# Kernel optimization log

Hardware: AMD Instinct MI355X
Metric: run time of the kernel (lower is better)

Reference implementation:

```python
import jax, jax.numpy as jnp
import numpy as np


def setup_inputs() -> dict:
    key = jax.random.key(0)
    ks = jax.random.split(key, 16)
    B, P, ENC = 128, 196, 2048          # batch, num pixels (14x14), encoder feature size
    E = D = A = 512                      # embed, decoder(hidden), attention sizes
    V, L = 10000, 52                     # vocab, max caption length
    s = 0.02
    rn = lambda k, shp: jax.random.normal(k, shp, jnp.float32) * s
    return {
        "features": jax.random.normal(ks[0], (B, P, ENC), jnp.float32),
        "captions": jax.random.randint(ks[1], (B, L), 0, V),
        "caption_lengths": jax.random.randint(ks[2], (B, 1), 2, L + 1),
        "emb": jax.random.uniform(ks[3], (V, E), jnp.float32, -0.1, 0.1),
        "W_enc_att": rn(ks[4], (ENC, A)), "b_enc_att": jnp.zeros((A,), jnp.float32),
        "W_dec_att": rn(ks[5], (D, A)),   "b_dec_att": jnp.zeros((A,), jnp.float32),
        "w_full": rn(ks[6], (A,)),        "b_full": jnp.zeros((), jnp.float32),
        "W_h0": rn(ks[7], (ENC, D)),      "b_h0": jnp.zeros((D,), jnp.float32),
        "W_c0": rn(ks[8], (ENC, D)),      "b_c0": jnp.zeros((D,), jnp.float32),
        "W_beta": rn(ks[9], (D, ENC)),    "b_beta": jnp.zeros((ENC,), jnp.float32),
        "W_ih": rn(ks[10], (E + ENC, 4 * D)), "b_ih": jnp.zeros((4 * D,), jnp.float32),
        "W_hh": rn(ks[11], (D, 4 * D)),       "b_hh": jnp.zeros((4 * D,), jnp.float32),
        "W_fc": jax.random.uniform(ks[12], (D, V), jnp.float32, -0.1, 0.1),
        "b_fc": jnp.zeros((V,), jnp.float32),
    }


def reference(features, captions, caption_lengths, emb,
              W_enc_att, b_enc_att, W_dec_att, b_dec_att, w_full, b_full,
              W_h0, b_h0, W_c0, b_c0, W_beta, b_beta,
              W_ih, b_ih, W_hh, b_hh, W_fc, b_fc):
    lens = caption_lengths[:, 0]
    order = jnp.argsort(-lens)                       # sort descending by length (stable)
    features = features[order]
    captions = captions[order]
    decode_lengths = lens[order] - 1                 # [B]
    T = captions.shape[1] - 1                        # static max decode length

    emb_seq = emb[captions[:, :T]]                   # [B,T,E]
    eo = features.mean(axis=1)                       # [B,ENC]
    h = eo @ W_h0 + b_h0                             # [B,D]
    c = eo @ W_c0 + b_c0
    enc_proj = features @ W_enc_att + b_enc_att      # [B,P,A] (precomputed, h-independent)

    def step(carry, xs):
        h, c = carry
        t, e_t = xs                                  # e_t: [B,E]
        mask = (decode_lengths > t)[:, None].astype(h.dtype)  # rows still decoding
        dec_proj = h @ W_dec_att + b_dec_att         # [B,A]
        scores = jax.nn.relu(enc_proj + dec_proj[:, None, :]) @ w_full + b_full  # [B,P]
        alpha = jax.nn.softmax(scores, axis=-1)      # [B,P]
        attw = jnp.einsum('bp,bpe->be', alpha, features)       # attention-weighted enc
        gate = jax.nn.sigmoid(h @ W_beta + b_beta)   # [B,ENC]
        x = jnp.concatenate([e_t, gate * attw], axis=1)        # [B,E+ENC]
        gates = x @ W_ih + b_ih + h @ W_hh + b_hh    # [B,4D], torch LSTMCell order i,f,g,o
        i, f, g, o = jnp.split(gates, 4, axis=1)
        c_new = jax.nn.sigmoid(f) * c + jax.nn.sigmoid(i) * jnp.tanh(g)
        h_new = jax.nn.sigmoid(o) * jnp.tanh(c_new)
        preds = h_new @ W_fc + b_fc                  # dropout is identity in eval
        h = mask * h_new + (1.0 - mask) * h          # freeze finished rows
        c = mask * c_new + (1.0 - mask) * c
        return (h, c), (preds * mask, alpha * mask)

    (_, _), (preds, alphas) = jax.lax.scan(
        step, (h, c), (jnp.arange(T), jnp.swapaxes(emb_seq, 0, 1)))
    predictions = jnp.swapaxes(preds, 0, 1)          # [B,T,V]
    alphas = jnp.swapaxes(alphas, 0, 1)              # [B,T,P]
    return predictions, captions, decode_lengths, alphas
```

## Files before the change

kernel.cpp:

```cpp
#include <hip/hip_runtime.h>
#include <math.h>

#define NB 128
#define NP 196
#define NENC 2048
#define NE 512
#define ND 512
#define NA 512
#define NV 10000
#define NVPAD 10112
#define NL 52
#define NT 51
#define KXH2 2560

typedef unsigned short u16;
typedef __attribute__((ext_vector_type(8))) short bf16x8;
typedef __attribute__((ext_vector_type(8))) unsigned short u16x8;
typedef __attribute__((ext_vector_type(4))) float f32x4;

#define MFMA16 __builtin_amdgcn_mfma_f32_16x16x32_bf16

__device__ __forceinline__ float sigmoidf_(float v) { return 1.0f / (1.0f + __expf(-v)); }
__device__ __forceinline__ float b2f(u16 u) { return __uint_as_float(((unsigned int)u) << 16); }
__device__ __forceinline__ u16 f2b(float f) {
  unsigned int u = __float_as_uint(f);
  unsigned int r = (u + 0x7FFFu + ((u >> 16) & 1u)) >> 16;
  return (u16)r;
}

__global__ void kSort(const int* __restrict__ cap_len, const int* __restrict__ captions,
                      int* __restrict__ order, int* __restrict__ nact,
                      float* __restrict__ out_cap, float* __restrict__ out_dlen) {
  __shared__ int lens[NB];
  __shared__ int s_dl[NB];
  int tid = threadIdx.x;
  lens[tid] = cap_len[tid];
  __syncthreads();
  int li = lens[tid];
  int r = 0;
  for (int j = 0; j < NB; ++j) {
    int lj = lens[j];
    if (lj > li || (lj == li && j < tid)) r++;
  }
  order[r] = tid;
  s_dl[r] = li - 1;
  out_dlen[r] = (float)(li - 1);
  for (int l = 0; l < NL; ++l)
    out_cap[(size_t)r * NL + l] = (float)captions[(size_t)tid * NL + l];
  __syncthreads();
  if (tid < NT) {
    int cnt = 0;
    for (int j = 0; j < NB; ++j) cnt += (s_dl[j] > tid) ? 1 : 0;
    nact[tid] = cnt;
  }
}

__global__ void kAlphaZero(const int* __restrict__ nact, float* __restrict__ out_alph) {
  int t = blockIdx.x;
  int n0 = nact[t];
  int cnt = (NB - n0) * NP;
  for (int i = threadIdx.x; i < cnt; i += 256) {
    int b = n0 + i / NP;
    int p = i - (i / NP) * NP;
    out_alph[((size_t)b * NT + t) * NP + p] = 0.0f;
  }
}

__global__ void kFeats(const float* __restrict__ features, const int* __restrict__ order,
                       u16* __restrict__ featsb) {
  int p = blockIdx.x, b = blockIdx.y, tid = threadIdx.x;
  const float* src = features + ((size_t)order[b] * NP + p) * NENC + tid * 8;
  u16* dst = featsb + ((size_t)b * NP + p) * NENC + tid * 8;
  float4 v0 = *(const float4*)src;
  float4 v1 = *(const float4*)(src + 4);
  u16x8 o;
  o[0] = f2b(v0.x); o[1] = f2b(v0.y); o[2] = f2b(v0.z); o[3] = f2b(v0.w);
  o[4] = f2b(v1.x); o[5] = f2b(v1.y); o[6] = f2b(v1.z); o[7] = f2b(v1.w);
  *(u16x8*)dst = o;
}

__device__ __forceinline__ float tfetch(int mode, int k, int n,
                                        const float* __restrict__ A,
                                        const float* __restrict__ B) {
  switch (mode) {
    case 0: return A[(size_t)k * NA + n];
    case 1: return (n < NA) ? A[(size_t)k * NA + n] : B[(size_t)k * NENC + (n - NA)];
    case 2: return A[(size_t)k * (4 * ND) + (n & 3) * ND + (n >> 2)];
    case 3: {
      int col = (n & 3) * ND + (n >> 2);
      return (k < NENC) ? A[(size_t)(NE + k) * (4 * ND) + col]
                        : B[(size_t)(k - NENC) * (4 * ND) + col];
    }
    case 4: return (n < NV) ? A[(size_t)k * NV + n] : 0.0f;
    default: return (n < NA) ? A[(size_t)k * ND + n] : B[(size_t)k * ND + (n - NA)];
  }
}

__global__ __launch_bounds__(256) void kTrans(const float* __restrict__ A,
                                              const float* __restrict__ B,
                                              u16* __restrict__ dst,
                                              int K, int N, int mode) {
  __shared__ u16 T[32][136];
  int n0 = blockIdx.x * 32, k0 = blockIdx.y * 128;
  int tid = threadIdx.x;
  int c = tid & 31, kr = tid >> 5;
#pragma unroll
  for (int pass = 0; pass < 16; ++pass) {
    int kl = pass * 8 + kr;
    T[c][kl] = f2b(tfetch(mode, k0 + kl, n0 + c, A, B));
  }
  __syncthreads();
  int row = tid >> 3, seg = tid & 7;
  u16x8 v0, v1;
#pragma unroll
  for (int j = 0; j < 8; ++j) { v0[j] = T[row][seg * 16 + j]; v1[j] = T[row][seg * 16 + 8 + j]; }
  *(u16x8*)&dst[(size_t)(n0 + row) * K + k0 + seg * 16] = v0;
  *(u16x8*)&dst[(size_t)(n0 + row) * K + k0 + seg * 16 + 8] = v1;
}

__global__ void kEmbA(const float* __restrict__ emb, const int* __restrict__ captions,
                      const int* __restrict__ order, u16* __restrict__ embA) {
  int t = blockIdx.x, b = blockIdx.y;
  int tok = captions[(size_t)order[b] * NL + t];
  int i = threadIdx.x * 2;
  float2 v = *(const float2*)(emb + (size_t)tok * NE + i);
  unsigned int w0 = (unsigned int)f2b(v.x) | ((unsigned int)f2b(v.y) << 16);
  *(unsigned int*)(embA + ((size_t)t * NB + b) * NE + i) = w0;
}

__global__ __launch_bounds__(256) void kEmbGemm(const u16* __restrict__ A,
                                                const u16* __restrict__ BT,
                                                u16* __restrict__ D) {
  int w = threadIdx.x >> 6, lane = threadIdx.x & 63;
  int lr = lane & 15, lg = lane >> 4;
  int mb = blockIdx.y * 128 + w * 32;
  int nb = blockIdx.x * 64;
  f32x4 acc[2][4] = {};
  const u16* a0 = A + (size_t)(mb + lr) * NE + lg * 8;
  const u16* a1 = a0 + 16 * NE;
  const u16* b0 = BT + (size_t)(nb + lr) * NE + lg * 8;
  for (int k0 = 0; k0 < NE; k0 += 32) {
    bf16x8 af0 = *(const bf16x8*)(a0 + k0);
    bf16x8 af1 = *(const bf16x8*)(a1 + k0);
#pragma unroll
    for (int nt = 0; nt < 4; ++nt) {
      bf16x8 bf = *(const bf16x8*)(b0 + (size_t)nt * 16 * NE + k0);
      acc[0][nt] = MFMA16(af0, bf, acc[0][nt], 0, 0, 0);
      acc[1][nt] = MFMA16(af1, bf, acc[1][nt], 0, 0, 0);
    }
  }
#pragma unroll
  for (int mt = 0; mt < 2; ++mt)
#pragma unroll
    for (int nt = 0; nt < 4; ++nt)
#pragma unroll
      for (int j = 0; j < 4; ++j) {
        int row = mb + mt * 16 + lg * 4 + j;
        int col = nb + nt * 16 + lr;
        D[(size_t)row * NENC + col] = f2b(acc[mt][nt][j]);
      }
}

__global__ void kEo(const u16* __restrict__ featsb, u16* __restrict__ eob) {
  int e = blockIdx.x * 256 + threadIdx.x;
  int b = blockIdx.y;
  const u16* f = featsb + (size_t)b * NP * NENC + e;
  float s = 0.0f;
  for (int p = 0; p < NP; ++p) s += b2f(f[(size_t)p * NENC]);
  eob[(size_t)b * NENC + e] = f2b(s * (1.0f / NP));
}

__global__ __launch_bounds__(64) void kHC0(const u16* __restrict__ eob,
                                           const u16* __restrict__ BT,
                                           const float* __restrict__ b_h0,
                                           const float* __restrict__ b_c0,
                                           u16* __restrict__ hb, u16* __restrict__ xh0,
                                           float* __restrict__ c) {
  int lane = threadIdx.x;
  int lr = lane & 15, lg = lane >> 4;
  int mb = blockIdx.y * 32, nb = blockIdx.x * 32;
  f32x4 acc[2][2] = {};
  const u16* a0 = eob + (size_t)(mb + lr) * NENC + lg * 8;
  const u16* a1 = a0 + 16 * NENC;
  const u16* b0 = BT + (size_t)(nb + lr) * NENC + lg * 8;
  const u16* b1 = b0 + 16 * NENC;
#pragma unroll 4
  for (int k0 = 0; k0 < NENC; k0 += 32) {
    bf16x8 af0 = *(const bf16x8*)(a0 + k0);
    bf16x8 af1 = *(const bf16x8*)(a1 + k0);
    bf16x8 bv0 = *(const bf16x8*)(b0 + k0);
    bf16x8 bv1 = *(const bf16x8*)(b1 + k0);
    acc[0][0] = MFMA16(af0, bv0, acc[0][0], 0, 0, 0);
    acc[1][0] = MFMA16(af1, bv0, acc[1][0], 0, 0, 0);
    acc[0][1] = MFMA16(af0, bv1, acc[0][1], 0, 0, 0);
    acc[1][1] = MFMA16(af1, bv1, acc[1][1], 0, 0, 0);
  }
#pragma unroll
  for (int mt = 0; mt < 2; ++mt)
#pragma unroll
    for (int nt = 0; nt < 2; ++nt)
#pragma unroll
      for (int j = 0; j < 4; ++j) {
        int row = mb + mt * 16 + lg * 4 + j;
        int n = nb + nt * 16 + lr;
        if (n < NA) {
          u16 hv = f2b(acc[mt][nt][j] + b_h0[n]);
          hb[(size_t)row * ND + n] = hv;
          xh0[(size_t)row * KXH2 + NENC + n] = hv;
        } else {
          c[(size_t)row * ND + (n - NA)] = acc[mt][nt][j] + b_c0[n - NA];
        }
      }
}

__global__ __launch_bounds__(256) void kEncProj(const u16* __restrict__ A,
                                                const u16* __restrict__ BT,
                                                const float* __restrict__ bias,
                                                u16* __restrict__ D) {
  __shared__ u16 As[2][128][72];
  int bid = blockIdx.x;
  int mt = bid >> 2, ntile = bid & 3;
  int mb = mt * 128, nb = ntile * 128;
  int tid = threadIdx.x;
  int w = tid >> 6, lane = tid & 63;
  int lr = lane & 15, lg = lane >> 4;

  int arow[4], akp[4];
  const u16* aptr[4];
#pragma unroll
  for (int i = 0; i < 4; ++i) {
    int idx = i * 256 + tid;
    arow[i] = idx >> 3;
    akp[i] = idx & 7;
    aptr[i] = A + (size_t)(mb + arow[i]) * NENC + akp[i] * 8;
  }
  u16x8 s0 = *(const u16x8*)(aptr[0]);
  u16x8 s1 = *(const u16x8*)(aptr[1]);
  u16x8 s2 = *(const u16x8*)(aptr[2]);
  u16x8 s3 = *(const u16x8*)(aptr[3]);
  *(u16x8*)&As[0][arow[0]][akp[0] * 8] = s0;
  *(u16x8*)&As[0][arow[1]][akp[1] * 8] = s1;
  *(u16x8*)&As[0][arow[2]][akp[2] * 8] = s2;
  *(u16x8*)&As[0][arow[3]][akp[3] * 8] = s3;

  f32x4 acc[2][8] = {};
  const u16* bbase = BT + (size_t)(nb + lr) * NENC + lg * 8;
  int cur = 0;
  int r0 = w * 32 + lr;

  for (int k0 = 0; k0 < NENC; k0 += 64) {
    __syncthreads();
    bool more = (k0 + 64 < NENC);
    if (more) {
      s0 = *(const u16x8*)(aptr[0] + k0 + 64);
      s1 = *(const u16x8*)(aptr[1] + k0 + 64);
      s2 = *(const u16x8*)(aptr[2] + k0 + 64);
      s3 = *(const u16x8*)(aptr[3] + k0 + 64);
    }
#pragma unroll
    for (int kh = 0; kh < 2; ++kh) {
      bf16x8 af0 = *(const bf16x8*)&As[cur][r0][kh * 32 + lg * 8];
      bf16x8 af1 = *(const bf16x8*)&As[cur][r0 + 16][kh * 32 + lg * 8];
#pragma unroll
      for (int nt = 0; nt < 8; ++nt) {
        bf16x8 bf = *(const bf16x8*)(bbase + (size_t)nt * 16 * NENC + k0 + kh * 32);
        acc[0][nt] = MFMA16(af0, bf, acc[0][nt], 0, 0, 0);
        acc[1][nt] = MFMA16(af1, bf, acc[1][nt], 0, 0, 0);
      }
    }
    if (more) {
      *(u16x8*)&As[cur ^ 1][arow[0]][akp[0] * 8] = s0;
      *(u16x8*)&As[cur ^ 1][arow[1]][akp[1] * 8] = s1;
      *(u16x8*)&As[cur ^ 1][arow[2]][akp[2] * 8] = s2;
      *(u16x8*)&As[cur ^ 1][arow[3]][akp[3] * 8] = s3;
    }
    cur ^= 1;
  }
  __syncthreads();
  u16* eps = (u16*)As;
#pragma unroll
  for (int m2 = 0; m2 < 2; ++m2)
#pragma unroll
    for (int nt = 0; nt < 8; ++nt)
#pragma unroll
      for (int j = 0; j < 4; ++j) {
        int rloc = w * 32 + m2 * 16 + lg * 4 + j;
        int col = nt * 16 + lr;
        eps[rloc * 136 + col] = f2b(acc[m2][nt][j] + bias[nb + col]);
      }
  __syncthreads();
#pragma unroll
  for (int i = 0; i < 8; ++i) {
    int idx = i * 256 + tid;
    int row = idx >> 4, seg = idx & 15;
    *(u16x8*)&D[(size_t)(mb + row) * NA + nb + seg * 8] = *(u16x8*)&eps[row * 136 + seg * 8];
  }
}

__global__ __launch_bounds__(64) void kDecGate(const u16* __restrict__ hb,
                                               const u16* __restrict__ BT,
                                               const float* __restrict__ b_dec,
                                               const float* __restrict__ b_beta,
                                               const int* __restrict__ nact, int t,
                                               float* __restrict__ dec_proj,
                                               float* __restrict__ gate_raw) {
  int nact_t = nact[t];
  int mb = blockIdx.y * 32;
  if (mb >= nact_t) return;
  int lane = threadIdx.x;
  int lr = lane & 15, lg = lane >> 4;
  int nb = blockIdx.x * 32;
  f32x4 acc[2][2] = {};
  const u16* a0 = hb + (size_t)(mb + lr) * ND + lg * 8;
  const u16* a1 = a0 + 16 * ND;
  const u16* b0 = BT + (size_t)(nb + lr) * ND + lg * 8;
  const u16* b1 = b0 + 16 * ND;
#pragma unroll 4
  for (int k0 = 0; k0 < ND; k0 += 32) {
    bf16x8 af0 = *(const bf16x8*)(a0 + k0);
    bf16x8 af1 = *(const bf16x8*)(a1 + k0);
    bf16x8 bv0 = *(const bf16x8*)(b0 + k0);
    bf16x8 bv1 = *(const bf16x8*)(b1 + k0);
    acc[0][0] = MFMA16(af0, bv0, acc[0][0], 0, 0, 0);
    acc[1][0] = MFMA16(af1, bv0, acc[1][0], 0, 0, 0);
    acc[0][1] = MFMA16(af0, bv1, acc[0][1], 0, 0, 0);
    acc[1][1] = MFMA16(af1, bv1, acc[1][1], 0, 0, 0);
  }
#pragma unroll
  for (int mt = 0; mt < 2; ++mt)
#pragma unroll
    for (int nt = 0; nt < 2; ++nt)
#pragma unroll
      for (int j = 0; j < 4; ++j) {
        int row = mb + mt * 16 + lg * 4 + j;
        int n = nb + nt * 16 + lr;
        if (n < NA)
          dec_proj[(size_t)row * NA + n] = acc[mt][nt][j] + b_dec[n];
        else
          gate_raw[(size_t)row * NENC + (n - NA)] = acc[mt][nt][j] + b_beta[n - NA];
      }
}

__global__ __launch_bounds__(256) void kSAX(const u16* __restrict__ featsb,
                                            const u16* __restrict__ encb,
                                            const float* __restrict__ dec_proj,
                                            const float* __restrict__ gate_raw,
                                            const float* __restrict__ w_full,
                                            const float* __restrict__ b_full,
                                            const int* __restrict__ nact, int t,
                                            u16* __restrict__ xh_w,
                                            float* __restrict__ out_alph) {
  int b = blockIdx.x, r = blockIdx.y, tid = threadIdx.x;
  if (b >= nact[t]) return;
  __shared__ float s_dp[NA], s_wf[NA], s_al[NP + 12], red[16];
  for (int i = tid; i < NA; i += 256) { s_dp[i] = dec_proj[(size_t)b * NA + i]; s_wf[i] = w_full[i]; }
  __syncthreads();
  int wave = tid >> 6, lane = tid & 63;
  float bf_ = b_full[0];
  for (int p = wave; p < NP; p += 4) {
    const u16* ep = encb + ((size_t)b * NP + p) * NA + lane * 8;
    u16x8 v = *(const u16x8*)ep;
    float acc = 0.0f;
#pragma unroll
    for (int j = 0; j < 8; ++j) {
      int a = lane * 8 + j;
      float vv = b2f(v[j]) + s_dp[a];
      acc += fmaxf(vv, 0.0f) * s_wf[a];
    }
#pragma unroll
    for (int off = 32; off; off >>= 1) acc += __shfl_down(acc, off);
    if (lane == 0) s_al[p] = acc + bf_;
  }
  __syncthreads();
  float mx = -3.4e38f;
  for (int p = tid; p < NP; p += 256) mx = fmaxf(mx, s_al[p]);
#pragma unroll
  for (int off = 32; off; off >>= 1) mx = fmaxf(mx, __shfl_down(mx, off));
  if (lane == 0) red[wave] = mx;
  __syncthreads();
  if (tid == 0) red[0] = fmaxf(fmaxf(red[0], red[1]), fmaxf(red[2], red[3]));
  __syncthreads();
  float m2v = red[0];
  float sm = 0.0f;
  for (int p = tid; p < NP; p += 256) { float e = __expf(s_al[p] - m2v); s_al[p] = e; sm += e; }
#pragma unroll
  for (int off = 32; off; off >>= 1) sm += __shfl_down(sm, off);
  if (lane == 0) red[8 + wave] = sm;
  __syncthreads();
  if (tid == 0) red[8] = 1.0f / (red[8] + red[9] + red[10] + red[11]);
  __syncthreads();
  float inv = red[8];
  for (int p = tid; p < NP; p += 256) {
    float al = s_al[p] * inv;
    s_al[p] = al;
    if (r == 0) out_alph[((size_t)b * NT + t) * NP + p] = al;
  }
  __syncthreads();
  int e0 = r * 512 + tid * 2;
  float ac0 = 0.0f, ac1 = 0.0f;
  const u16* fb = featsb + (size_t)b * NP * NENC + e0;
#pragma unroll 4
  for (int p = 0; p < NP; ++p) {
    unsigned int v = *(const unsigned int*)(fb + (size_t)p * NENC);
    float al = s_al[p];
    ac0 += al * __uint_as_float(v << 16);
    ac1 += al * __uint_as_float(v & 0xffff0000u);
  }
  float g0 = sigmoidf_(gate_raw[(size_t)b * NENC + e0]);
  float g1 = sigmoidf_(gate_raw[(size_t)b * NENC + e0 + 1]);
  unsigned int wo = (unsigned int)f2b(ac0 * g0) | ((unsigned int)f2b(ac1 * g1) << 16);
  *(unsigned int*)(xh_w + (size_t)b * KXH2 + e0) = wo;
}

__global__ __launch_bounds__(1024) void kGatesLstm(const u16* __restrict__ xh_r,
                                                   const u16* __restrict__ WifgoT2,
                                                   const u16* __restrict__ embAll,
                                                   const float* __restrict__ b_ih,
                                                   const float* __restrict__ b_hh,
                                                   const int* __restrict__ nact, int t,
                                                   float* __restrict__ cst,
                                                   u16* __restrict__ hb,
                                                   u16* __restrict__ hnewAll_t,
                                                   u16* __restrict__ xh_w) {
  __shared__ float smem[8 * 32 * 33];
  int nact_t = nact[t];
  int tid = threadIdx.x;
  int w = tid >> 6, lane = tid & 63;
  int lr = lane & 15, lg = lane >> 4;
  int rt = blockIdx.x & 3, ct = blockIdx.x >> 2;
  int mb = rt * 32, nb = ct * 32;
  int kq = w >> 1, mh = w & 1;
  if (mb < nact_t) {
    f32x4 acc0 = {}, acc1 = {};
    const u16* pa = xh_r + (size_t)(mb + mh * 16 + lr) * KXH2 + kq * 320 + lg * 8;
    const u16* pb0 = WifgoT2 + (size_t)(nb + lr) * KXH2 + kq * 320 + lg * 8;
    const u16* pb1 = pb0 + (size_t)16 * KXH2;
#pragma unroll
    for (int k0 = 0; k0 < 320; k0 += 32) {
      bf16x8 af = *(const bf16x8*)(pa + k0);
      bf16x8 bv0 = *(const bf16x8*)(pb0 + k0);
      bf16x8 bv1 = *(const bf16x8*)(pb1 + k0);
      acc0 = MFMA16(af, bv0, acc0, 0, 0, 0);
      acc1 = MFMA16(af, bv1, acc1, 0, 0, 0);
    }
#pragma unroll
    for (int j = 0; j < 4; ++j) {
      int rr = kq * 32 + mh * 16 + lg * 4 + j;
      smem[rr * 33 + lr] = acc0[j];
      smem[rr * 33 + 16 + lr] = acc1[j];
    }
  }
  __syncthreads();
  if (tid < 256) {
    int row = tid >> 3, dl = tid & 7;
    int grow = mb + row;
    int d = ct * 8 + dl;
    size_t off = (size_t)grow * ND + d;
    if (grow < nact_t) {
      float g4[4];
#pragma unroll
      for (int g = 0; g < 4; ++g) {
        int col = dl * 4 + g;
        float s = 0.0f;
#pragma unroll
        for (int q = 0; q < 8; ++q) s += smem[(q * 32 + row) * 33 + col];
        s += b2f(embAll[((size_t)t * NB + grow) * NENC + nb + col]);
        g4[g] = s;
      }
      float gi = g4[0] + b_ih[d] + b_hh[d];
      float gf = g4[1] + b_ih[ND + d] + b_hh[ND + d];
      float gg = g4[2] + b_ih[2 * ND + d] + b_hh[2 * ND + d];
      float go = g4[3] + b_ih[3 * ND + d] + b_hh[3 * ND + d];
      float cn = sigmoidf_(gf) * cst[off] + sigmoidf_(gi) * tanhf(gg);
      float hn = sigmoidf_(go) * tanhf(cn);
      u16 hv = f2b(hn);
      cst[off] = cn;
      hb[off] = hv;
      hnewAll_t[off] = hv;
      xh_w[(size_t)grow * KXH2 + NENC + d] = hv;
    } else {
      xh_w[(size_t)grow * KXH2 + NENC + d] = hb[off];
    }
  }
}

__global__ __launch_bounds__(256) void kPredsAll3(const u16* __restrict__ hnewAll,
                                                  const u16* __restrict__ BT,
                                                  const float* __restrict__ b_fc,
                                                  const int* __restrict__ nact,
                                                  float* __restrict__ out_pred) {
  __shared__ float ts[128][68];
  int t = blockIdx.x;
  int nb = blockIdx.y * 64;
  int nact_t = nact[t];
  int w = threadIdx.x >> 6, lane = threadIdx.x & 63;
  int lr = lane & 15, lg = lane >> 4;
  int mb = w * 32;
  f32x4 acc[2][4] = {};
  if (mb < nact_t) {
    const u16* a0 = hnewAll + (size_t)t * NB * ND + (size_t)(mb + lr) * ND + lg * 8;
    const u16* a1 = a0 + 16 * ND;
    const u16* b0 = BT + (size_t)(nb + lr) * ND + lg * 8;
    for (int k0 = 0; k0 < ND; k0 += 32) {
      bf16x8 af0 = *(const bf16x8*)(a0 + k0);
      bf16x8 af1 = *(const bf16x8*)(a1 + k0);
#pragma unroll
      for (int nt = 0; nt < 4; ++nt) {
        bf16x8 bf = *(const bf16x8*)(b0 + (size_t)nt * 16 * ND + k0);
        acc[0][nt] = MFMA16(af0, bf, acc[0][nt], 0, 0, 0);
        acc[1][nt] = MFMA16(af1, bf, acc[1][nt], 0, 0, 0);
      }
    }
  }
#pragma unroll
  for (int mt = 0; mt < 2; ++mt)
#pragma unroll
    for (int nt = 0; nt < 4; ++nt)
#pragma unroll
      for (int j = 0; j < 4; ++j) {
        int row = mb + mt * 16 + lg * 4 + j;
        int gn = nb + nt * 16 + lr;
        float bias = (gn < NV) ? b_fc[gn] : 0.0f;
        ts[row][nt * 16 + lr] = (row < nact_t) ? (acc[mt][nt][j] + bias) : 0.0f;
      }
  __syncthreads();
  int tid = threadIdx.x;
#pragma unroll
  for (int i = 0; i < 8; ++i) {
    int idx = i * 256 + tid;
    int row = idx >> 4;
    int c4 = (idx & 15) * 4;
    int gn = nb + c4;
    if (gn < NV) {
      f32x4 v = *(const f32x4*)&ts[row][c4];
      __builtin_nontemporal_store(v, (f32x4*)&out_pred[((size_t)row * NT + t) * NV + gn]);
    }
  }
}

extern "C" void kernel_launch(void* const* d_in, const int* in_sizes, int n_in,
                              void* d_out, int out_size, void* d_ws, size_t ws_size,
                              hipStream_t stream) {
  (void)in_sizes; (void)n_in; (void)out_size; (void)ws_size;
  const float* features  = (const float*)d_in[0];
  const int*   captions  = (const int*)d_in[1];
  const int*   cap_len   = (const int*)d_in[2];
  const float* emb       = (const float*)d_in[3];
  const float* W_enc_att = (const float*)d_in[4];
  const float* b_enc_att = (const float*)d_in[5];
  const float* W_dec_att = (const float*)d_in[6];
  const float* b_dec_att = (const float*)d_in[7];
  const float* w_full    = (const float*)d_in[8];
  const float* b_full    = (const float*)d_in[9];
  const float* W_h0      = (const float*)d_in[10];
  const float* b_h0      = (const float*)d_in[11];
  const float* W_c0      = (const float*)d_in[12];
  const float* b_c0      = (const float*)d_in[13];
  const float* W_beta    = (const float*)d_in[14];
  const float* b_beta    = (const float*)d_in[15];
  const float* W_ih      = (const float*)d_in[16];
  const float* b_ih      = (const float*)d_in[17];
  const float* W_hh      = (const float*)d_in[18];
  const float* b_hh      = (const float*)d_in[19];
  const float* W_fc      = (const float*)d_in[20];
  const float* b_fc      = (const float*)d_in[21];

  float* out      = (float*)d_out;
  float* out_pred = out;
  float* out_cap  = out_pred + (size_t)NB * NT * NV;
  float* out_dlen = out_cap + (size_t)NB * NL;
  float* out_alph = out_dlen + NB;

  char* p = (char*)d_ws;
  auto alloc = [&](size_t nbytes) { void* r = (void*)p; p += (nbytes + 255) & ~(size_t)255; return r; };
  int*   order    = (int*)alloc(NB * 4);
  int*   nact     = (int*)alloc(NT * 4);
  u16*   eob      = (u16*)alloc((size_t)NB * NENC * 2);
  float* c        = (float*)alloc((size_t)NB * ND * 4);
  u16*   hb       = (u16*)alloc((size_t)NB * ND * 2);
  u16*   xh0      = (u16*)alloc((size_t)NB * KXH2 * 2);
  u16*   xh1      = (u16*)alloc((size_t)NB * KXH2 * 2);
  u16*   hnewAll  = (u16*)alloc((size_t)NT * NB * ND * 2);
  float* dec_proj = (float*)alloc((size_t)NB * NA * 4);
  float* gate_raw = (float*)alloc((size_t)NB * NENC * 4);
  u16*   featsb   = (u16*)alloc((size_t)NB * NP * NENC * 2);
  u16*   encb     = (u16*)alloc((size_t)NB * NP * NA * 2);
  u16*   WencT    = (u16*)alloc((size_t)NA * NENC * 2);
  u16*   WdgT     = (u16*)alloc((size_t)(NA + NENC) * ND * 2);
  u16*   WihTopT  = (u16*)alloc((size_t)NENC * NE * 2);
  u16*   WifgoT2  = (u16*)alloc((size_t)NENC * KXH2 * 2);
  u16*   WfcT     = (u16*)alloc((size_t)NVPAD * ND * 2);
  u16*   WhcT     = (u16*)alloc((size_t)1024 * NENC * 2);
  u16*   embA     = (u16*)alloc((size_t)NT * NB * NE * 2);
  u16*   embAll   = (u16*)alloc((size_t)NT * NB * NENC * 2);

  kSort<<<1, NB, 0, stream>>>(cap_len, captions, order, nact, out_cap, out_dlen);
  kAlphaZero<<<NT, 256, 0, stream>>>(nact, out_alph);
  kFeats<<<dim3(NP, NB), 256, 0, stream>>>(features, order, featsb);
  kTrans<<<dim3(512 / 32, 2048 / 128), 256, 0, stream>>>(W_enc_att, nullptr, WencT, 2048, 512, 0);
  kTrans<<<dim3(2560 / 32, 512 / 128), 256, 0, stream>>>(W_dec_att, W_beta, WdgT, 512, 2560, 1);
  kTrans<<<dim3(2048 / 32, 512 / 128), 256, 0, stream>>>(W_ih, nullptr, WihTopT, 512, 2048, 2);
  kTrans<<<dim3(2048 / 32, 2560 / 128), 256, 0, stream>>>(W_ih, W_hh, WifgoT2, 2560, 2048, 3);
  kTrans<<<dim3(NVPAD / 32, 512 / 128), 256, 0, stream>>>(W_fc, nullptr, WfcT, 512, NVPAD, 4);
  kTrans<<<dim3(1024 / 32, 2048 / 128), 256, 0, stream>>>(W_h0, W_c0, WhcT, 2048, 1024, 5);
  kEmbA<<<dim3(NT, NB), 256, 0, stream>>>(emb, captions, order, embA);
  kEmbGemm<<<dim3(NENC / 64, NT), 256, 0, stream>>>(embA, WihTopT, embAll);
  kEo<<<dim3(NENC / 256, NB), 256, 0, stream>>>(featsb, eob);
  kHC0<<<dim3(1024 / 32, NB / 32), 64, 0, stream>>>(eob, WhcT, b_h0, b_c0, hb, xh0, c);
  kEncProj<<<784, 256, 0, stream>>>(featsb, WencT, b_enc_att, encb);

  for (int t = 0; t < NT; ++t) {
    u16* xh_r = (t & 1) ? xh1 : xh0;
    u16* xh_w = (t & 1) ? xh0 : xh1;
    kDecGate<<<dim3((NA + NENC) / 32, 4), 64, 0, stream>>>(hb, WdgT, b_dec_att, b_beta,
                                                           nact, t, dec_proj, gate_raw);
    kSAX<<<dim3(NB, 4), 256, 0, stream>>>(featsb, encb, dec_proj, gate_raw, w_full, b_full,
                                          nact, t, xh_r, out_alph);
    kGatesLstm<<<256, 1024, 0, stream>>>(xh_r, WifgoT2, embAll, b_ih, b_hh, nact, t,
                                         c, hb, hnewAll + (size_t)t * NB * ND, xh_w);
  }
  kPredsAll3<<<dim3(NT, NVPAD / 64), 256, 0, stream>>>(hnewAll, WfcT, b_fc, nact, out_pred);
}
```

Measured before the change: 4.511 ms.

## Widen LSTM gate tiles and skip writing inactive prediction rows

Measured after the change: 4.750 ms. 1.05x slower.

```diff
diff --git a/kernel.cpp b/kernel.cpp
--- a/kernel.cpp
+++ b/kernel.cpp
@@ -30,6 +30,7 @@
 
 __global__ void kSort(const int* __restrict__ cap_len, const int* __restrict__ captions,
                       int* __restrict__ order, int* __restrict__ nact,
+                      int* __restrict__ dlen_sorted,
                       float* __restrict__ out_cap, float* __restrict__ out_dlen) {
   __shared__ int lens[NB];
   __shared__ int s_dl[NB];
@@ -44,6 +45,7 @@
   }
   order[r] = tid;
   s_dl[r] = li - 1;
+  dlen_sorted[r] = li - 1;
   out_dlen[r] = (float)(li - 1);
   for (int l = 0; l < NL; ++l)
     out_cap[(size_t)r * NL + l] = (float)captions[(size_t)tid * NL + l];
@@ -64,6 +66,19 @@
     int p = i - (i / NP) * NP;
     out_alph[((size_t)b * NT + t) * NP + p] = 0.0f;
   }
+}
+
+__global__ __launch_bounds__(256) void kPredTail(const int* __restrict__ dlen_sorted,
+                                                 float* __restrict__ out_pred) {
+  int row = blockIdx.x;
+  int d = dlen_sorted[row];
+  int cnt = (NT - d) * NV;
+  float* base = out_pred + (size_t)row * NT * NV + (size_t)d * NV;
+  f32x4 z = {0.0f, 0.0f, 0.0f, 0.0f};
+  int start = (blockIdx.y * 256 + threadIdx.x) * 4;
+  int step = gridDim.y * 256 * 4;
+  for (int i = start; i < cnt; i += step)
+    __builtin_nontemporal_store(z, (f32x4*)&base[i]);
 }
 
 __global__ void kFeats(const float* __restrict__ features, const int* __restrict__ order,
@@ -422,39 +437,44 @@
                                                    u16* __restrict__ hb,
                                                    u16* __restrict__ hnewAll_t,
                                                    u16* __restrict__ xh_w) {
-  __shared__ float smem[8 * 32 * 33];
+  __shared__ float smem[8][32][68];
   int nact_t = nact[t];
   int tid = threadIdx.x;
   int w = tid >> 6, lane = tid & 63;
   int lr = lane & 15, lg = lane >> 4;
   int rt = blockIdx.x & 3, ct = blockIdx.x >> 2;
-  int mb = rt * 32, nb = ct * 32;
-  int kq = w >> 1, mh = w & 1;
+  int mb = rt * 32, nb = ct * 64;
+  int kq = w >> 1, nh = w & 1;
   if (mb < nact_t) {
-    f32x4 acc0 = {}, acc1 = {};
-    const u16* pa = xh_r + (size_t)(mb + mh * 16 + lr) * KXH2 + kq * 320 + lg * 8;
-    const u16* pb0 = WifgoT2 + (size_t)(nb + lr) * KXH2 + kq * 320 + lg * 8;
+    f32x4 acc[2][2] = {};
+    const u16* pa0 = xh_r + (size_t)(mb + lr) * KXH2 + kq * 320 + lg * 8;
+    const u16* pa1 = pa0 + (size_t)16 * KXH2;
+    const u16* pb0 = WifgoT2 + (size_t)(nb + nh * 32 + lr) * KXH2 + kq * 320 + lg * 8;
     const u16* pb1 = pb0 + (size_t)16 * KXH2;
 #pragma unroll
     for (int k0 = 0; k0 < 320; k0 += 32) {
-      bf16x8 af = *(const bf16x8*)(pa + k0);
+      bf16x8 a0 = *(const bf16x8*)(pa0 + k0);
+      bf16x8 a1 = *(const bf16x8*)(pa1 + k0);
       bf16x8 bv0 = *(const bf16x8*)(pb0 + k0);
       bf16x8 bv1 = *(const bf16x8*)(pb1 + k0);
-      acc0 = MFMA16(af, bv0, acc0, 0, 0, 0);
-      acc1 = MFMA16(af, bv1, acc1, 0, 0, 0);
-    }
-#pragma unroll
-    for (int j = 0; j < 4; ++j) {
-      int rr = kq * 32 + mh * 16 + lg * 4 + j;
-      smem[rr * 33 + lr] = acc0[j];
-      smem[rr * 33 + 16 + lr] = acc1[j];
-    }
-  }
-  __syncthreads();
-  if (tid < 256) {
-    int row = tid >> 3, dl = tid & 7;
+      acc[0][0] = MFMA16(a0, bv0, acc[0][0], 0, 0, 0);
+      acc[1][0] = MFMA16(a1, bv0, acc[1][0], 0, 0, 0);
+      acc[0][1] = MFMA16(a0, bv1, acc[0][1], 0, 0, 0);
+      acc[1][1] = MFMA16(a1, bv1, acc[1][1], 0, 0, 0);
+    }
+#pragma unroll
+    for (int mt = 0; mt < 2; ++mt)
+#pragma unroll
+      for (int nt = 0; nt < 2; ++nt)
+#pragma unroll
+        for (int j = 0; j < 4; ++j)
+          smem[kq][mt * 16 + lg * 4 + j][nh * 32 + nt * 16 + lr] = acc[mt][nt][j];
+  }
+  __syncthreads();
+  if (tid < 512) {
+    int row = tid >> 4, dl = tid & 15;
     int grow = mb + row;
-    int d = ct * 8 + dl;
+    int d = ct * 16 + dl;
     size_t off = (size_t)grow * ND + d;
     if (grow < nact_t) {
       float g4[4];
@@ -463,7 +483,7 @@
         int col = dl * 4 + g;
         float s = 0.0f;
 #pragma unroll
-        for (int q = 0; q < 8; ++q) s += smem[(q * 32 + row) * 33 + col];
+        for (int q = 0; q < 8; ++q) s += smem[q][row][col];
         s += b2f(embAll[((size_t)t * NB + grow) * NENC + nb + col]);
         g4[g] = s;
       }
@@ -484,7 +504,7 @@
   }
 }
 
-__global__ __launch_bounds__(256) void kPredsAll3(const u16* __restrict__ hnewAll,
+__global__ __launch_bounds__(256) void kPredsAll4(const u16* __restrict__ hnewAll,
                                                   const u16* __restrict__ BT,
                                                   const float* __restrict__ b_fc,
                                                   const int* __restrict__ nact,
@@ -521,7 +541,7 @@
         int row = mb + mt * 16 + lg * 4 + j;
         int gn = nb + nt * 16 + lr;
         float bias = (gn < NV) ? b_fc[gn] : 0.0f;
-        ts[row][nt * 16 + lr] = (row < nact_t) ? (acc[mt][nt][j] + bias) : 0.0f;
+        ts[row][nt * 16 + lr] = acc[mt][nt][j] + bias;
       }
   __syncthreads();
   int tid = threadIdx.x;
@@ -531,7 +551,7 @@
     int row = idx >> 4;
     int c4 = (idx & 15) * 4;
     int gn = nb + c4;
-    if (gn < NV) {
+    if (row < nact_t && gn < NV) {
       f32x4 v = *(const f32x4*)&ts[row][c4];
       __builtin_nontemporal_store(v, (f32x4*)&out_pred[((size_t)row * NT + t) * NV + gn]);
     }
@@ -575,6 +595,7 @@
   auto alloc = [&](size_t nbytes) { void* r = (void*)p; p += (nbytes + 255) & ~(size_t)255; return r; };
   int*   order    = (int*)alloc(NB * 4);
   int*   nact     = (int*)alloc(NT * 4);
+  int*   dlen_s   = (int*)alloc(NB * 4);
   u16*   eob      = (u16*)alloc((size_t)NB * NENC * 2);
   float* c        = (float*)alloc((size_t)NB * ND * 4);
   u16*   hb       = (u16*)alloc((size_t)NB * ND * 2);
@@ -594,8 +615,9 @@
   u16*   embA     = (u16*)alloc((size_t)NT * NB * NE * 2);
   u16*   embAll   = (u16*)alloc((size_t)NT * NB * NENC * 2);
 
-  kSort<<<1, NB, 0, stream>>>(cap_len, captions, order, nact, out_cap, out_dlen);
+  kSort<<<1, NB, 0, stream>>>(cap_len, captions, order, nact, dlen_s, out_cap, out_dlen);
   kAlphaZero<<<NT, 256, 0, stream>>>(nact, out_alph);
+  kPredTail<<<dim3(NB, 16), 256, 0, stream>>>(dlen_s, out_pred);
   kFeats<<<dim3(NP, NB), 256, 0, stream>>>(features, order, featsb);
   kTrans<<<dim3(512 / 32, 2048 / 128), 256, 0, stream>>>(W_enc_att, nullptr, WencT, 2048, 512, 0);
   kTrans<<<dim3(2560 / 32, 512 / 128), 256, 0, stream>>>(W_dec_att, W_beta, WdgT, 512, 2560, 1);
@@ -616,8 +638,8 @@
                                                            nact, t, dec_proj, gate_raw);
     kSAX<<<dim3(NB, 4), 256, 0, stream>>>(featsb, encb, dec_proj, gate_raw, w_full, b_full,
                                           nact, t, xh_r, out_alph);
-    kGatesLstm<<<256, 1024, 0, stream>>>(xh_r, WifgoT2, embAll, b_ih, b_hh, nact, t,
+    kGatesLstm<<<128, 1024, 0, stream>>>(xh_r, WifgoT2, embAll, b_ih, b_hh, nact, t,
                                          c, hb, hnewAll + (size_t)t * NB * ND, xh_w);
   }
-  kPredsAll3<<<dim3(NT, NVPAD / 64), 256, 0, stream>>>(hnewAll, WfcT, b_fc, nact, out_pred);
-}
+  kPredsAll4<<<dim3(NT, NVPAD / 64), 256, 0, stream>>>(hnewAll, WfcT, b_fc, nact, out_pred);
+}
```
